# Performance work log

Hardware: AMD Instinct MI355X
Metric: run time of the kernel (lower is better)

Reference implementation:

```python
import jax, jax.numpy as jnp
import numpy as np

N = 100000      # nodes
E = 1600000     # edges (avg degree 16)
IN_C = 128
HID = 64
OUT_C = 2


def compute_norm(edge_index, n):
    """1/rowcount of M = I + A^T (distinct nonzeros per row, coalesce semantics)."""
    idt = edge_index.dtype
    ar = jnp.arange(n, dtype=idt)
    rows = jnp.concatenate([ar, edge_index[1]])  # M built from transposed edges
    cols = jnp.concatenate([ar, edge_index[0]])
    order = jnp.lexsort((cols, rows))
    rs, cs = rows[order], cols[order]
    uniq = jnp.concatenate([jnp.array([True]),
                            (rs[1:] != rs[:-1]) | (cs[1:] != cs[:-1])])
    rowcount = jnp.zeros((n,), jnp.float32).at[rs].add(uniq.astype(jnp.float32))
    return 1.0 / jnp.maximum(rowcount, 1.0)


def pan_conv(x, edge_index, w_lin, b_lin, w_pan, norm):
    # PyG PANConv, filter_size=1: out = diag(norm) @ (w0*I + w0*w1*A^T) @ (x W + b)
    h = x @ w_lin + b_lin                                   # [N, HID]
    src, dst = edge_index[0], edge_index[1]
    agg = jnp.zeros_like(h).at[dst].add(h[src])             # (A^T h)[i] = sum_{src->i} h[src]
    out = w_pan[0] * h + (w_pan[0] * w_pan[1]) * agg
    return norm[:, None] * out


def setup_inputs() -> dict:
    key = jax.random.key(0)
    ks = jax.random.split(key, 8)
    x = jax.random.normal(ks[0], (N, IN_C), jnp.float32)
    edge_index = jax.random.randint(ks[1], (2, E), 0, N, dtype=jnp.int32)
    w1_lin = jax.random.normal(ks[2], (IN_C, HID), jnp.float32) * 0.05
    b1_lin = jnp.zeros((HID,), jnp.float32)
    w1_pan = jax.random.uniform(ks[3], (2,), jnp.float32, 0.5, 1.5)
    w2_lin = jax.random.normal(ks[4], (HID, HID), jnp.float32) * 0.05
    b2_lin = jnp.zeros((HID,), jnp.float32)
    w2_pan = jax.random.uniform(ks[5], (2,), jnp.float32, 0.5, 1.5)
    wc = jax.random.normal(ks[6], (2 * HID, OUT_C), jnp.float32) * 0.05
    bc = jnp.zeros((OUT_C,), jnp.float32)
    return {"x": x, "edge_index": edge_index,
            "w1_lin": w1_lin, "b1_lin": b1_lin, "w1_pan": w1_pan,
            "w2_lin": w2_lin, "b2_lin": b2_lin, "w2_pan": w2_pan,
            "wc": wc, "bc": bc}


def reference(x, edge_index, w1_lin, b1_lin, w1_pan, w2_lin, b2_lin, w2_pan, wc, bc):
    n = x.shape[0]
    norm = compute_norm(edge_index, n)          # graph-structure only; shared by both layers
    h = pan_conv(x, edge_index, w1_lin, b1_lin, w1_pan, norm)
    h = jax.nn.relu(h)
    h = pan_conv(h, edge_index, w2_lin, b2_lin, w2_pan, norm)
    row, col = edge_index[0], edge_index[1]
    emb = jnp.concatenate([h[row], h[col]], axis=-1)  # [E, 2*HID]
    return emb @ wc + bc                               # [E, OUT_C]
```

## Files before the change

kernel.cpp:

```cpp
#include <hip/hip_runtime.h>
#include <hip/hip_bf16.h>

#define NNODES 100000
#define NEDGES 1600000
#define INC 128
#define HIDC 64
#define BSHIFT 8
#define NB ((NNODES + 255) / 256)
#define TILE 8192
#define HSLOTS 8192
#define CAP 8192
#define CAPE 8192
#define NBLK_FILL ((NEDGES + TILE - 1) / TILE)
#define NBLK_LIN ((NNODES + 63) / 64)

typedef short bf16x8 __attribute__((ext_vector_type(8)));
typedef float f32x4 __attribute__((ext_vector_type(4)));

__device__ __forceinline__ float bf2f(unsigned short h) {
    return __uint_as_float((unsigned)h << 16);
}
__device__ __forceinline__ unsigned short f2bf(float f) {
    __hip_bfloat16 h = __float2bfloat16(f);
    return *(unsigned short*)&h;
}

__global__ __launch_bounds__(256) void prep_w_kernel(
        const float* __restrict__ w1, unsigned short* __restrict__ wTh,
        unsigned short* __restrict__ wTl,
        const float* __restrict__ w2_lin, const float* __restrict__ b2,
        const float* __restrict__ wc, float* __restrict__ w44,
        float* __restrict__ bias4, unsigned short* __restrict__ out) {
    int t = threadIdx.x;
    int e = blockIdx.x * 256 + t;
    int c = e >> 7, k = e & 127;
    float v = w1[k * 64 + c];
    unsigned short hi = f2bf(v);
    wTh[e] = hi;
    wTl[e] = f2bf(v - bf2f(hi));
    if (blockIdx.x == 0) {
        if (t < 16)
            *(ushort4*)(out + (size_t)NNODES * 64 + t * 4) = make_ushort4(0, 0, 0, 0);
        int kk = t >> 2, j = t & 3;
        float a = 0.0f;
#pragma unroll 8
        for (int i = 0; i < 64; i++) {
            float w4 = (j < 2) ? wc[i * 2 + j] : wc[(64 + i) * 2 + (j - 2)];
            a += w2_lin[kk * 64 + i] * w4;
        }
        w44[kk * 4 + j] = a;
        if (kk == 0) {
            float bb4 = 0.0f;
            for (int i = 0; i < 64; i++) {
                float w4 = (j < 2) ? wc[i * 2 + j] : wc[(64 + i) * 2 + (j - 2)];
                bb4 += b2[i] * w4;
            }
            bias4[j] = bb4;
        }
    }
}

__global__ __launch_bounds__(256) void fat_kernel(
        const float* __restrict__ x,
        const unsigned short* __restrict__ wTh, const unsigned short* __restrict__ wTl,
        const float* __restrict__ b, unsigned short* __restrict__ out,
        const int* __restrict__ src, const int* __restrict__ dst,
        int* __restrict__ bucket_fill, unsigned int* __restrict__ staging) {
    __shared__ alignas(16) unsigned short s_a[2][64 * 128];
    __shared__ alignas(16) unsigned short s_b[2][64 * 128];
    int t = threadIdx.x;
    if (blockIdx.x < NBLK_FILL) {
        int* cnt = (int*)&s_a[0][0];
        int* basepos = cnt + NB;
        unsigned int* svl = (unsigned int*)&s_b[0][0];
        for (int i = t; i < NB; i += 256) cnt[i] = 0;
        __syncthreads();
        int tile0 = blockIdx.x * TILE;
        int meta[32];
#pragma unroll
        for (int i = 0; i < 32; i++) {
            int e = tile0 + i * 256 + t;
            meta[i] = -1;
            if (e < NEDGES) {
                int s = src[e], d = dst[e];
                int bkt = d >> BSHIFT;
                int r = atomicAdd(&cnt[bkt], 1);
                meta[i] = (bkt << 13) | r;
                svl[i * 256 + t] = ((unsigned)(d & 255) << 17) | (unsigned)s;
            }
        }
        __syncthreads();
        for (int i = t; i < NB; i += 256) {
            int c = cnt[i];
            int g = (c > 0) ? atomicAdd(&bucket_fill[i], c) : 0;
            basepos[i] = (i << 13) + g;
        }
        __syncthreads();
#pragma unroll
        for (int i = 0; i < 32; i++) {
            if (meta[i] >= 0) {
                int bkt = meta[i] >> 13, r = meta[i] & 8191;
                staging[basepos[bkt] + r] = svl[i * 256 + t];
            }
        }
    } else {
        int node0 = (blockIdx.x - NBLK_FILL) * 64;
        float4 vx[8];
#pragma unroll
        for (int it = 0; it < 8; it++) {
            int idx = it * 256 + t;
            int row = idx >> 5, c4 = idx & 31;
            int node = node0 + row;
            if (node < NNODES)
                vx[it] = *(const float4*)(x + (size_t)node * INC + c4 * 4);
            else
                vx[it] = make_float4(0.f, 0.f, 0.f, 0.f);
        }
        uint4 vwh[4], vwl[4];
#pragma unroll
        for (int j = 0; j < 4; j++) {
            vwh[j] = *(const uint4*)(wTh + (size_t)(j * 256 + t) * 8);
            vwl[j] = *(const uint4*)(wTl + (size_t)(j * 256 + t) * 8);
        }
#pragma unroll
        for (int it = 0; it < 8; it++) {
            int idx = it * 256 + t;
            int row = idx >> 5, c4 = idx & 31;
            ushort4 hi, lo;
            hi.x = f2bf(vx[it].x); lo.x = f2bf(vx[it].x - bf2f(hi.x));
            hi.y = f2bf(vx[it].y); lo.y = f2bf(vx[it].y - bf2f(hi.y));
            hi.z = f2bf(vx[it].z); lo.z = f2bf(vx[it].z - bf2f(hi.z));
            hi.w = f2bf(vx[it].w); lo.w = f2bf(vx[it].w - bf2f(hi.w));
            int ke = (c4 * 4) ^ ((row & 7) << 3);
            *(ushort4*)&s_a[0][row * 128 + ke] = hi;
            *(ushort4*)&s_a[1][row * 128 + ke] = lo;
        }
#pragma unroll
        for (int j = 0; j < 4; j++) {
            int idx = j * 256 + t;
            int col = idx >> 4, k0 = (idx & 15) * 8;
            int ke = k0 ^ ((col & 7) << 3);
            *(uint4*)&s_b[0][col * 128 + ke] = vwh[j];
            *(uint4*)&s_b[1][col * 128 + ke] = vwl[j];
        }
        __syncthreads();
        int l = t & 63, wv = t >> 6;
        int mr = l & 15, g = l >> 4;
        int arow = wv * 16 + mr;
        f32x4 acc[4] = {{0.f, 0.f, 0.f, 0.f}, {0.f, 0.f, 0.f, 0.f},
                        {0.f, 0.f, 0.f, 0.f}, {0.f, 0.f, 0.f, 0.f}};
#pragma unroll
        for (int ks = 0; ks < 4; ks++) {
            int k0 = ks * 32 + g * 8;
            int ko = k0 ^ ((mr & 7) << 3);
            bf16x8 ah = *(const bf16x8*)&s_a[0][arow * 128 + ko];
            bf16x8 al = *(const bf16x8*)&s_a[1][arow * 128 + ko];
#pragma unroll
            for (int cb = 0; cb < 4; cb++) {
                int bo = (cb * 16 + mr) * 128 + ko;
                bf16x8 bh = *(const bf16x8*)&s_b[0][bo];
                bf16x8 bl = *(const bf16x8*)&s_b[1][bo];
                acc[cb] = __builtin_amdgcn_mfma_f32_16x16x32_bf16(ah, bh, acc[cb], 0, 0, 0);
                acc[cb] = __builtin_amdgcn_mfma_f32_16x16x32_bf16(ah, bl, acc[cb], 0, 0, 0);
                acc[cb] = __builtin_amdgcn_mfma_f32_16x16x32_bf16(al, bh, acc[cb], 0, 0, 0);
            }
        }
#pragma unroll
        for (int cb = 0; cb < 4; cb++) {
            int col = cb * 16 + mr;
            float bb = b[col];
#pragma unroll
            for (int r = 0; r < 4; r++) {
                int node = node0 + wv * 16 + g * 4 + r;
                if (node < NNODES)
                    out[(size_t)node * 64 + col] = f2bf(acc[cb][r] + bb);
            }
        }
    }
}

__global__ __launch_bounds__(256) void fill2_kernel(
        const int* __restrict__ bucket_fill, const unsigned int* __restrict__ staging,
        int* __restrict__ csr_src, int* __restrict__ row_start,
        int* __restrict__ row_pdeg, float* __restrict__ norm, int n_nodes) {
    __shared__ int cnt[256];
    __shared__ int dcount[256];
    __shared__ int off[256];
    __shared__ int pscan[256];
    __shared__ unsigned short rank16[CAP];
    __shared__ unsigned int ht[HSLOTS];
    int t = threadIdx.x;
    int b = blockIdx.x;
    int node0 = b << BSHIFT;
    int nn = min(256, n_nodes - node0);
    cnt[t] = 0; dcount[t] = 0;
    {
        uint4* h4 = (uint4*)ht;
        uint4 ff = make_uint4(0xFFFFFFFFu, 0xFFFFFFFFu, 0xFFFFFFFFu, 0xFFFFFFFFu);
        for (int i = t; i < HSLOTS / 4; i += 256) h4[i] = ff;
    }
    __syncthreads();
    int start = b << 13;
    int total = bucket_fill[b];
    for (int li = t; li < total; li += 256) {
        unsigned int w = staging[start + li];
        int s = (int)(w & 0x1FFFFu);
        int dl = (int)(w >> 17);
        int r = atomicAdd(&cnt[dl], 1);
        rank16[li] = (unsigned short)r;
        if (s != node0 + dl) {
            unsigned int slot = ((w * 2654435761u) >> 13) & (HSLOTS - 1);
            while (true) {
                unsigned int prev = atomicCAS(&ht[slot], 0xFFFFFFFFu, w);
                if (prev == 0xFFFFFFFFu) { atomicAdd(&dcount[dl], 1); break; }
                if (prev == w) break;
                slot = (slot + 1) & (HSLOTS - 1);
            }
        }
    }
    __syncthreads();
    int cv = cnt[t];
    int pv = (cv + 7) & ~7;
    pscan[t] = pv;
    __syncthreads();
    for (int o = 1; o < 256; o <<= 1) {
        int xx = (t >= o) ? pscan[t - o] : 0;
        __syncthreads();
        pscan[t] += xx;
        __syncthreads();
    }
    off[t] = b * CAPE + pscan[t] - pv;
    __syncthreads();
    if (t < nn) {
        row_start[node0 + t] = off[t];
        row_pdeg[node0 + t] = pv;
        norm[node0 + t] = 1.0f / (1.0f + (float)dcount[t]);
    }
    for (int k = cv; k < pv; k++) csr_src[off[t] + k] = n_nodes;
    for (int li = t; li < total; li += 256) {
        unsigned int w = staging[start + li];
        int s = (int)(w & 0x1FFFFu);
        int dl = (int)(w >> 17);
        csr_src[off[dl] + (int)rank16[li]] = s;
    }
}

__global__ void agg_h_kernel(const unsigned int* __restrict__ lin32,
                             const int* __restrict__ row_start,
                             const int* __restrict__ row_pdeg,
                             const int* __restrict__ csr_src,
                             const float* __restrict__ norm,
                             const float* __restrict__ wpan, const float* __restrict__ w44,
                             const float* __restrict__ bias4, float* __restrict__ u,
                             int n_nodes) {
    int t = threadIdx.x;
    int node = blockIdx.x * 4 + (t >> 6);
    int lane = t & 63;
    int sl = lane & 31;
    int h5 = lane >> 5;
    if (blockIdx.x == 0 && t < 4) u[n_nodes * 4 + t] = 0.0f;
    if (node >= n_nodes) return;
    int e0 = row_start[node];
    int pd = row_pdeg[node];
    float aLo0 = 0.f, aHi0 = 0.f, aLo1 = 0.f, aHi1 = 0.f;
    for (int base = 0; base < pd; base += 64) {
        int sidx = csr_src[e0 + base + lane];
        int m = min(64, pd - base);
        for (int p = 0; p < m; p += 8) {
#pragma unroll
            for (int pp = 0; pp < 8; pp += 4) {
                int sA0 = __builtin_amdgcn_readlane(sidx, p + pp + 0);
                int sB0 = __builtin_amdgcn_readlane(sidx, p + pp + 1);
                int sA1 = __builtin_amdgcn_readlane(sidx, p + pp + 2);
                int sB1 = __builtin_amdgcn_readlane(sidx, p + pp + 3);
                int s0 = h5 ? sB0 : sA0;
                int s1 = h5 ? sB1 : sA1;
                unsigned int wd0 = lin32[(size_t)s0 * 32 + sl];
                unsigned int wd1 = lin32[(size_t)s1 * 32 + sl];
                aLo0 += __uint_as_float(wd0 << 16);
                aHi0 += __uint_as_float(wd0 & 0xFFFF0000u);
                aLo1 += __uint_as_float(wd1 << 16);
                aHi1 += __uint_as_float(wd1 & 0xFFFF0000u);
            }
        }
    }
    float accLo = aLo0 + aLo1;
    float accHi = aHi0 + aHi1;
    accLo += __shfl_xor(accLo, 32);
    accHi += __shfl_xor(accHi, 32);
    unsigned int wself = lin32[(size_t)node * 32 + sl];
    float nr = norm[node];
    float w0 = wpan[0];
    float w01 = wpan[0] * wpan[1];
    float vLo = fmaxf(nr * (w0 * __uint_as_float(wself << 16) + w01 * accLo), 0.0f);
    float vHi = fmaxf(nr * (w0 * __uint_as_float(wself & 0xFFFF0000u) + w01 * accHi), 0.0f);
    int c0 = 2 * sl;
    float4 wv0 = *(const float4*)(w44 + c0 * 4);
    float4 wv1 = *(const float4*)(w44 + (c0 + 1) * 4);
    float p0 = vLo * wv0.x + vHi * wv1.x;
    float p1 = vLo * wv0.y + vHi * wv1.y;
    float p2 = vLo * wv0.z + vHi * wv1.z;
    float p3 = vLo * wv0.w + vHi * wv1.w;
    for (int off = 16; off; off >>= 1) {
        p0 += __shfl_xor(p0, off);
        p1 += __shfl_xor(p1, off);
        p2 += __shfl_xor(p2, off);
        p3 += __shfl_xor(p3, off);
    }
    if (lane == 0) {
        float4 bb = *(const float4*)bias4;
        *(float4*)(u + node * 4) =
            make_float4(p0 + bb.x, p1 + bb.y, p2 + bb.z, p3 + bb.w);
    }
}

__global__ void agg_pq4_kernel(const float* __restrict__ u, const int* __restrict__ row_start,
                               const int* __restrict__ row_pdeg,
                               const int* __restrict__ csr_src,
                               const float* __restrict__ norm,
                               const float* __restrict__ wpan, float* __restrict__ pq,
                               int n_nodes) {
    int t = threadIdx.x;
    int node = blockIdx.x * 64 + (t >> 2);
    int j = t & 3;
    if (node >= n_nodes) return;
    int e0 = row_start[node];
    int pd = row_pdeg[node];
    float acc = 0.0f;
    for (int e = 0; e < pd; e += 8) {
#pragma unroll
        for (int k = 0; k < 8; k++) {
            int s = csr_src[e0 + e + k];
            acc += u[s * 4 + j];
        }
    }
    float w0 = wpan[0];
    float w01 = wpan[0] * wpan[1];
    pq[node * 4 + j] = norm[node] * (w0 * u[node * 4 + j] + w01 * acc);
}

__global__ void edge_out_kernel(const int* __restrict__ src, const int* __restrict__ dst,
                                const float* __restrict__ pq, const float* __restrict__ bc,
                                float* __restrict__ out, int n_edges) {
    int e = blockIdx.x * blockDim.x + threadIdx.x;
    if (e >= n_edges) return;
    int r = src[e], c = dst[e];
    float2 p = *(const float2*)(pq + r * 4);
    float2 q = *(const float2*)(pq + c * 4 + 2);
    float2 o = make_float2(p.x + q.x + bc[0], p.y + q.y + bc[1]);
    *(float2*)(out + e * 2) = o;
}

extern "C" void kernel_launch(void* const* d_in, const int* in_sizes, int n_in,
                              void* d_out, int out_size, void* d_ws, size_t ws_size,
                              hipStream_t stream) {
    const float* x      = (const float*)d_in[0];
    const int*   eidx   = (const int*)d_in[1];
    const float* w1_lin = (const float*)d_in[2];
    const float* b1_lin = (const float*)d_in[3];
    const float* w1_pan = (const float*)d_in[4];
    const float* w2_lin = (const float*)d_in[5];
    const float* b2_lin = (const float*)d_in[6];
    const float* w2_pan = (const float*)d_in[7];
    const float* wc     = (const float*)d_in[8];
    const float* bc     = (const float*)d_in[9];
    float* out = (float*)d_out;

    const int* src = eidx;
    const int* dst = eidx + NEDGES;

    char* ws = (char*)d_ws;
    size_t off = 0;
    auto carve = [&](size_t bytes) {
        char* p = ws + off;
        off = (off + bytes + 255) & ~(size_t)255;
        return p;
    };
    int*   bucket_fill = (int*)carve((size_t)NB * 4);
    int*   row_start = (int*)carve((size_t)NNODES * 4);
    int*   row_pdeg  = (int*)carve((size_t)NNODES * 4);
    unsigned int* staging = (unsigned int*)carve((size_t)NB * CAP * 4);
    int*   csr_src  = (int*)carve(((size_t)NB * CAPE + 256) * 4);
    float* nrm      = (float*)carve((size_t)NNODES * 4);
    unsigned short* bufA = (unsigned short*)carve((size_t)(NNODES + 1) * HIDC * 2);
    float* u        = (float*)carve((size_t)(NNODES + 1) * 4 * 4);
    float* pq       = (float*)carve((size_t)NNODES * 4 * 4);
    float* w44      = (float*)carve((size_t)64 * 4 * 4);
    float* bias4    = (float*)carve((size_t)4 * 4);
    unsigned short* wTh = (unsigned short*)carve((size_t)HIDC * INC * 2);
    unsigned short* wTl = (unsigned short*)carve((size_t)HIDC * INC * 2);
    (void)ws_size; (void)in_sizes; (void)n_in; (void)out_size;

    hipMemsetAsync(bucket_fill, 0, (size_t)NB * 4, stream);

    prep_w_kernel<<<32, 256, 0, stream>>>(w1_lin, wTh, wTl, w2_lin, b2_lin, wc,
                                          w44, bias4, bufA);

    fat_kernel<<<NBLK_FILL + NBLK_LIN, 256, 0, stream>>>(
        x, wTh, wTl, b1_lin, bufA, src, dst, bucket_fill, staging);

    fill2_kernel<<<NB, 256, 0, stream>>>(bucket_fill, staging, csr_src, row_start, row_pdeg,
                                         nrm, NNODES);

    agg_h_kernel<<<(NNODES + 3) / 4, 256, 0, stream>>>(
        (const unsigned int*)bufA, row_start, row_pdeg, csr_src, nrm, w1_pan, w44, bias4,
        u, NNODES);

    agg_pq4_kernel<<<(NNODES + 63) / 64, 256, 0, stream>>>(
        u, row_start, row_pdeg, csr_src, nrm, w2_pan, pq, NNODES);

    edge_out_kernel<<<NEDGES / 256, 256, 0, stream>>>(src, dst, pq, bc, out, NEDGES);
}
```

Baseline: 249.2 us.

## Process two nodes per wavefront in layer-1 aggregation with pre-scaled CSR offsets

```diff
diff --git a/kernel.cpp b/kernel.cpp
--- a/kernel.cpp
+++ b/kernel.cpp
@@ -236,12 +236,12 @@
         row_pdeg[node0 + t] = pv;
         norm[node0 + t] = 1.0f / (1.0f + (float)dcount[t]);
     }
-    for (int k = cv; k < pv; k++) csr_src[off[t] + k] = n_nodes;
+    for (int k = cv; k < pv; k++) csr_src[off[t] + k] = n_nodes << 7;
     for (int li = t; li < total; li += 256) {
         unsigned int w = staging[start + li];
         int s = (int)(w & 0x1FFFFu);
         int dl = (int)(w >> 17);
-        csr_src[off[dl] + (int)rank16[li]] = s;
+        csr_src[off[dl] + (int)rank16[li]] = s << 7;
     }
 }
 
@@ -254,29 +254,37 @@
                              const float* __restrict__ bias4, float* __restrict__ u,
                              int n_nodes) {
     int t = threadIdx.x;
-    int node = blockIdx.x * 4 + (t >> 6);
     int lane = t & 63;
     int sl = lane & 31;
     int h5 = lane >> 5;
+    int pair = blockIdx.x * 4 + (t >> 6);
+    int node = pair * 2 + h5;
     if (blockIdx.x == 0 && t < 4) u[n_nodes * 4 + t] = 0.0f;
-    if (node >= n_nodes) return;
-    int e0 = row_start[node];
-    int pd = row_pdeg[node];
+    if (pair * 2 >= n_nodes) return;
+    bool valid = (node < n_nodes);
+    int nc = valid ? node : 0;
+    int e0 = row_start[nc];
+    int pd = valid ? row_pdeg[nc] : 0;
+    int pmax = max(pd, __shfl_xor(pd, 32));
+    int sentB = n_nodes << 7;
+    unsigned sl4 = (unsigned)sl * 4;
+    const char* base8 = (const char*)lin32;
     float aLo0 = 0.f, aHi0 = 0.f, aLo1 = 0.f, aHi1 = 0.f;
-    for (int base = 0; base < pd; base += 64) {
-        int sidx = csr_src[e0 + base + lane];
-        int m = min(64, pd - base);
-        for (int p = 0; p < m; p += 8) {
-#pragma unroll
-            for (int pp = 0; pp < 8; pp += 4) {
-                int sA0 = __builtin_amdgcn_readlane(sidx, p + pp + 0);
-                int sB0 = __builtin_amdgcn_readlane(sidx, p + pp + 1);
-                int sA1 = __builtin_amdgcn_readlane(sidx, p + pp + 2);
-                int sB1 = __builtin_amdgcn_readlane(sidx, p + pp + 3);
-                int s0 = h5 ? sB0 : sA0;
-                int s1 = h5 ? sB1 : sA1;
-                unsigned int wd0 = lin32[(size_t)s0 * 32 + sl];
-                unsigned int wd1 = lin32[(size_t)s1 * 32 + sl];
+    for (int base = 0; base < pmax; base += 32) {
+        int li = base + sl;
+        int so = (li < pd) ? csr_src[e0 + li] : sentB;
+        int m = min(32, pmax - base);
+#pragma unroll
+        for (int i = 0; i < 32; i += 2) {
+            if (i < m) {
+                int sA0 = __builtin_amdgcn_readlane(so, i);
+                int sB0 = __builtin_amdgcn_readlane(so, 32 + i);
+                int sA1 = __builtin_amdgcn_readlane(so, i + 1);
+                int sB1 = __builtin_amdgcn_readlane(so, 33 + i);
+                int so0 = h5 ? sB0 : sA0;
+                int so1 = h5 ? sB1 : sA1;
+                unsigned int wd0 = *(const unsigned int*)(base8 + (unsigned)(so0 + sl4));
+                unsigned int wd1 = *(const unsigned int*)(base8 + (unsigned)(so1 + sl4));
                 aLo0 += __uint_as_float(wd0 << 16);
                 aHi0 += __uint_as_float(wd0 & 0xFFFF0000u);
                 aLo1 += __uint_as_float(wd1 << 16);
@@ -286,10 +294,8 @@
     }
     float accLo = aLo0 + aLo1;
     float accHi = aHi0 + aHi1;
-    accLo += __shfl_xor(accLo, 32);
-    accHi += __shfl_xor(accHi, 32);
-    unsigned int wself = lin32[(size_t)node * 32 + sl];
-    float nr = norm[node];
+    unsigned int wself = *(const unsigned int*)(base8 + (unsigned)((nc << 7) + sl4));
+    float nr = norm[nc];
     float w0 = wpan[0];
     float w01 = wpan[0] * wpan[1];
     float vLo = fmaxf(nr * (w0 * __uint_as_float(wself << 16) + w01 * accLo), 0.0f);
@@ -307,7 +313,7 @@
         p2 += __shfl_xor(p2, off);
         p3 += __shfl_xor(p3, off);
     }
-    if (lane == 0) {
+    if (sl == 0 && valid) {
         float4 bb = *(const float4*)bias4;
         *(float4*)(u + node * 4) =
             make_float4(p0 + bb.x, p1 + bb.y, p2 + bb.z, p3 + bb.w);
@@ -330,8 +336,8 @@
     for (int e = 0; e < pd; e += 8) {
 #pragma unroll
         for (int k = 0; k < 8; k++) {
-            int s = csr_src[e0 + e + k];
-            acc += u[s * 4 + j];
+            int so = csr_src[e0 + e + k];
+            acc += u[(so >> 5) + j];
         }
     }
     float w0 = wpan[0];
@@ -402,7 +408,7 @@
     fill2_kernel<<<NB, 256, 0, stream>>>(bucket_fill, staging, csr_src, row_start, row_pdeg,
                                          nrm, NNODES);
 
-    agg_h_kernel<<<(NNODES + 3) / 4, 256, 0, stream>>>(
+    agg_h_kernel<<<(NNODES + 7) / 8, 256, 0, stream>>>(
         (const unsigned int*)bufA, row_start, row_pdeg, csr_src, nrm, w1_pan, w44, bias4,
         u, NNODES);
 
```

Result: faster. 244.0 us (-2.1%).
